# Performance work log

Measured on AMD Instinct MI355X. Metric: run time of the kernel, lower is better.

## Reference

```python
import jax, jax.numpy as jnp
import numpy as np
import math

N_NODES = 100000
N_EDGES = 1600000
IN_DIM = 32
OUT_DIM = 32

def setup_inputs() -> dict:
    key = jax.random.key(0)
    k1, k2, k3, k4 = jax.random.split(key, 4)
    X = jax.random.normal(k1, (N_NODES, IN_DIM), dtype=jnp.float32)
    src_idx = jax.random.randint(k2, (N_EDGES,), 0, N_NODES, dtype=jnp.int64)
    dst_idx = jax.random.randint(k3, (N_EDGES,), 0, N_NODES, dtype=jnp.int64)
    # weights init: uniform(-stdv, stdv), stdv = 1/sqrt(output_dim)
    stdv = 1.0 / math.sqrt(OUT_DIM)
    W = jax.random.uniform(k4, (IN_DIM, OUT_DIM), dtype=jnp.float32,
                           minval=-stdv, maxval=stdv)
    return {"X": X, "W": W, "src_idx": src_idx, "dst_idx": dst_idx}

def reference(X, W, src_idx, dst_idx):
    # GIN sum-aggregation SpMM: agg[i] = sum_{j in N(i)} X[j]
    agg = jax.ops.segment_sum(X[src_idx], dst_idx, num_segments=N_NODES)
    # dense GEMM: X_prime = agg @ W
    return agg @ W
```

## Files before the change

kernel.cpp:

```cpp
#include <hip/hip_runtime.h>

#define N_DIM 32
#define NPB 64
#define NB_FINE_MAX 2048
#define CAPFINE 1280
#define CAPB 48
#define CEPB 16384
#define NSEG_MAX 128
#define FT 512
#define GROWS 512

__device__ __forceinline__ unsigned f2bf_rne(float f) {
    unsigned u = __float_as_uint(f);
    return (u + 0x7FFFu + ((u >> 16) & 1u)) >> 16;
}
__device__ __forceinline__ float bf2f(unsigned h) {
    return __uint_as_float(h << 16);
}

__global__ __launch_bounds__(FT) void k_fused(const float* __restrict__ X,
                                              const float* __restrict__ W,
                                              unsigned* __restrict__ Y,
                                              const int* __restrict__ src,
                                              const int* __restrict__ dst,
                                              int* __restrict__ cnt2,
                                              int* __restrict__ pairs2,
                                              int n_nodes, int n_edges,
                                              int nbins, int nblk_g) {
    __shared__ float Wlds[N_DIM * N_DIM];
    __shared__ int h[NB_FINE_MAX];
    const int t = threadIdx.x;

    if (blockIdx.x < nblk_g) {
        for (int i = t; i < N_DIM * N_DIM; i += FT) Wlds[i] = W[i];
        __syncthreads();
        const int r = blockIdx.x * GROWS + t;
        if (r >= n_nodes) return;

        float x[N_DIM];
        const float4* xr = (const float4*)(X + (size_t)r * N_DIM);
#pragma unroll
        for (int i = 0; i < N_DIM / 4; ++i) {
            float4 v = xr[i];
            x[4 * i + 0] = v.x; x[4 * i + 1] = v.y;
            x[4 * i + 2] = v.z; x[4 * i + 3] = v.w;
        }
        float acc[N_DIM];
#pragma unroll
        for (int c = 0; c < N_DIM; ++c) acc[c] = 0.0f;
#pragma unroll
        for (int k = 0; k < N_DIM; ++k) {
            const float xk = x[k];
#pragma unroll
            for (int c = 0; c < N_DIM; ++c)
                acc[c] = fmaf(xk, Wlds[k * N_DIM + c], acc[c]);
        }
        unsigned yp[16];
#pragma unroll
        for (int q = 0; q < 16; ++q)
            yp[q] = f2bf_rne(acc[2 * q]) | (f2bf_rne(acc[2 * q + 1]) << 16);
        uint4* yr = (uint4*)(Y + (size_t)r * 16);
#pragma unroll
        for (int i = 0; i < 4; ++i)
            yr[i] = make_uint4(yp[4 * i], yp[4 * i + 1],
                               yp[4 * i + 2], yp[4 * i + 3]);
    } else {
        for (int i = t; i < NB_FINE_MAX; i += FT) h[i] = 0;
        __syncthreads();
        const int seg = blockIdx.x - nblk_g;
        const int start = seg * CEPB;
        int* __restrict__ myseg = pairs2 + (size_t)seg * nbins * CAPB;

        for (int kb = 0; kb < CEPB / FT / 8; ++kb) {
            int vw[8], cw[8], rw[8];
#pragma unroll
            for (int k = 0; k < 8; ++k) {
                int e = start + t + (kb * 8 + k) * FT;
                if (e < n_edges) {
                    int d = dst[e];
                    cw[k] = d >> 6;
                    vw[k] = src[e] | ((d & 63) << 17);
                    rw[k] = atomicAdd(&h[cw[k]], 1);
                } else {
                    cw[k] = -1;
                }
            }
#pragma unroll
            for (int k = 0; k < 8; ++k)
                if (cw[k] >= 0 && rw[k] < CAPB)
                    myseg[cw[k] * CAPB + rw[k]] = vw[k];
        }
        __syncthreads();
        for (int i = t; i < nbins; i += FT)
            cnt2[(size_t)seg * nbins + i] = min(h[i], CAPB);
    }
}

__device__ __forceinline__ void addv(float* acc, uint4 v) {
    acc[0] += bf2f(v.x & 0xFFFFu); acc[1] += bf2f(v.x >> 16);
    acc[2] += bf2f(v.y & 0xFFFFu); acc[3] += bf2f(v.y >> 16);
    acc[4] += bf2f(v.z & 0xFFFFu); acc[5] += bf2f(v.z >> 16);
    acc[6] += bf2f(v.w & 0xFFFFu); acc[7] += bf2f(v.w >> 16);
}

__global__ __launch_bounds__(256) void k_agg(const uint4* __restrict__ Y4,
                                             const int* __restrict__ cnt2,
                                             const int* __restrict__ pairs2,
                                             float* __restrict__ out,
                                             int n_nodes, int nbins, int nseg) {
    __shared__ int qbuf[CAPFINE];
    __shared__ int sbin[CAPFINE];
    __shared__ int scnt[NSEG_MAX];
    __shared__ int soff[NSEG_MAX];
    __shared__ int slen;
    __shared__ int cnt[NPB];
    __shared__ int cst[NPB];
    __shared__ int excl[NPB];

    const int t = threadIdx.x;
    const int b = blockIdx.x;

    for (int i = t; i < NSEG_MAX; i += 256)
        scnt[i] = (i < nseg) ? cnt2[(size_t)i * nbins + b] : 0;
    __syncthreads();

    if (t < 64) {
        int a = scnt[t];
        int x = a;
#pragma unroll
        for (int o = 1; o < 64; o <<= 1) {
            int u = __shfl_up(x, o, 64);
            if (t >= o) x += u;
        }
        int b2 = scnt[64 + t];
        int y = b2;
#pragma unroll
        for (int o = 1; o < 64; o <<= 1) {
            int u = __shfl_up(y, o, 64);
            if (t >= o) y += u;
        }
        int tot1 = __shfl(x, 63, 64);
        int tot2 = __shfl(y, 63, 64);
        soff[t] = x - a;
        soff[64 + t] = tot1 + y - b2;
        if (t == 0) slen = tot1 + tot2;
    }
    __syncthreads();
    const int len = min(slen, CAPFINE);

    {
        const int w = t >> 6;
        const int lane = t & 63;
        for (int s = w; s < nseg; s += 4) {
            int c = scnt[s];
            if (lane < c) {
                int p = pairs2[((size_t)s * nbins + b) * CAPB + lane];
                int idx = soff[s] + lane;
                if (idx < CAPFINE) qbuf[idx] = p;
            }
        }
    }
    if (t < NPB) cnt[t] = 0;
    __syncthreads();

    int pv[CAPFINE / 256], rv[CAPFINE / 256];
#pragma unroll
    for (int k = 0; k < CAPFINE / 256; ++k) {
        int i = t + k * 256;
        if (i < len) {
            int p = qbuf[i];
            pv[k] = p;
            rv[k] = atomicAdd(&cnt[(p >> 17) & 63], 1);
        } else {
            pv[k] = -1;
        }
    }
    __syncthreads();
    if (t < 64) {
        int c0 = cnt[t];
        int c = c0;
#pragma unroll
        for (int off = 1; off < 64; off <<= 1) {
            int u = __shfl_up(c, off, 64);
            if (t >= off) c += u;
        }
        cst[t] = c;
        excl[t] = c - c0;
    }
    __syncthreads();
#pragma unroll
    for (int k = 0; k < CAPFINE / 256; ++k) {
        if (pv[k] >= 0) {
            int p = pv[k];
            sbin[excl[(p >> 17) & 63] + rv[k]] = p & 0x1FFFF;
        }
    }
    __syncthreads();

    const int g = t >> 2;
    const int l = t & 3;
    float acc[8];
#pragma unroll
    for (int i = 0; i < 8; ++i) acc[i] = 0.0f;

    const int s1 = cst[g];
    const int s0 = s1 - cnt[g];
    for (int e = s0; e < s1; e += 4) {
        const int m = s1 - e;
        int i0 = sbin[e];
        int i1 = sbin[e + ((m > 1) ? 1 : 0)];
        int i2 = sbin[e + ((m > 2) ? 2 : 0)];
        int i3 = sbin[e + ((m > 3) ? 3 : 0)];
        uint4 v0 = Y4[(size_t)i0 * 4 + l];
        uint4 v1 = Y4[(size_t)i1 * 4 + l];
        uint4 v2 = Y4[(size_t)i2 * 4 + l];
        uint4 v3 = Y4[(size_t)i3 * 4 + l];
        addv(acc, v0);
        if (m > 1) addv(acc, v1);
        if (m > 2) addv(acc, v2);
        if (m > 3) addv(acc, v3);
    }

    const int node = b * NPB + g;
    if (node < n_nodes) {
        ((float4*)out)[(size_t)node * 8 + 2 * l] =
            make_float4(acc[0], acc[1], acc[2], acc[3]);
        ((float4*)out)[(size_t)node * 8 + 2 * l + 1] =
            make_float4(acc[4], acc[5], acc[6], acc[7]);
    }
}

extern "C" void kernel_launch(void* const* d_in, const int* in_sizes, int n_in,
                              void* d_out, int out_size, void* d_ws, size_t ws_size,
                              hipStream_t stream) {
    const float* X   = (const float*)d_in[0];
    const float* W   = (const float*)d_in[1];
    const int*   src = (const int*)d_in[2];
    const int*   dst = (const int*)d_in[3];
    float* out = (float*)d_out;

    const int n_nodes = in_sizes[0] / N_DIM;
    const int n_edges = in_sizes[2];
    const int nbins = (n_nodes + NPB - 1) / NPB;
    const int nseg  = (n_edges + CEPB - 1) / CEPB;

    unsigned* Y  = (unsigned*)d_ws;
    int* cnt2    = (int*)(Y + (size_t)n_nodes * 16);
    int* pairs2  = cnt2 + (size_t)nseg * nbins;

    const int nblk_g = (n_nodes + GROWS - 1) / GROWS;

    k_fused<<<nblk_g + nseg, FT, 0, stream>>>(X, W, Y, src, dst, cnt2, pairs2,
                                              n_nodes, n_edges, nbins, nblk_g);
    k_agg<<<nbins, 256, 0, stream>>>((const uint4*)Y, cnt2, pairs2, out,
                                     n_nodes, nbins, nseg);
}
```

Baseline: 132.6 us.

## Shrink edge segments to raise binning parallelism and gather cells per thread

Edge segments shrink from 16384 to 4096 edges, with per-cell capacity cut from 48 to 16. The binning phase then launches four times as many blocks and each thread handles a single batch of 8 edges. The aggregation kernel now scans up to 512 segment counts in chunks and gathers each segment cell with one thread instead of one wave. This aims to spread the binning pass over more CUs, at the cost of more segment-count reads per bin in the aggregation kernel, serial per-thread gather loops, and a higher chance of cell overflow with capacity 16.

New measurement: 130.9 us. About the same (-1.3%).

```diff
diff --git a/kernel.cpp b/kernel.cpp
--- a/kernel.cpp
+++ b/kernel.cpp
@@ -4,9 +4,9 @@
 #define NPB 64
 #define NB_FINE_MAX 2048
 #define CAPFINE 1280
-#define CAPB 48
-#define CEPB 16384
-#define NSEG_MAX 128
+#define CAPB 16
+#define CEPB 4096
+#define NSEG_PAD 512
 #define FT 512
 #define GROWS 512
 
@@ -65,31 +65,29 @@
             yr[i] = make_uint4(yp[4 * i], yp[4 * i + 1],
                                yp[4 * i + 2], yp[4 * i + 3]);
     } else {
-        for (int i = t; i < NB_FINE_MAX; i += FT) h[i] = 0;
+        for (int i = t; i < nbins; i += FT) h[i] = 0;
         __syncthreads();
         const int seg = blockIdx.x - nblk_g;
         const int start = seg * CEPB;
         int* __restrict__ myseg = pairs2 + (size_t)seg * nbins * CAPB;
 
-        for (int kb = 0; kb < CEPB / FT / 8; ++kb) {
-            int vw[8], cw[8], rw[8];
-#pragma unroll
-            for (int k = 0; k < 8; ++k) {
-                int e = start + t + (kb * 8 + k) * FT;
-                if (e < n_edges) {
-                    int d = dst[e];
-                    cw[k] = d >> 6;
-                    vw[k] = src[e] | ((d & 63) << 17);
-                    rw[k] = atomicAdd(&h[cw[k]], 1);
-                } else {
-                    cw[k] = -1;
-                }
+        int vw[CEPB / FT], cw[CEPB / FT], rw[CEPB / FT];
+#pragma unroll
+        for (int k = 0; k < CEPB / FT; ++k) {
+            int e = start + t + k * FT;
+            if (e < n_edges) {
+                int d = dst[e];
+                cw[k] = d >> 6;
+                vw[k] = src[e] | ((d & 63) << 17);
+                rw[k] = atomicAdd(&h[cw[k]], 1);
+            } else {
+                cw[k] = -1;
             }
-#pragma unroll
-            for (int k = 0; k < 8; ++k)
-                if (cw[k] >= 0 && rw[k] < CAPB)
-                    myseg[cw[k] * CAPB + rw[k]] = vw[k];
-        }
+        }
+#pragma unroll
+        for (int k = 0; k < CEPB / FT; ++k)
+            if (cw[k] >= 0 && rw[k] < CAPB)
+                myseg[(size_t)cw[k] * CAPB + rw[k]] = vw[k];
         __syncthreads();
         for (int i = t; i < nbins; i += FT)
             cnt2[(size_t)seg * nbins + i] = min(h[i], CAPB);
@@ -110,8 +108,8 @@
                                              int n_nodes, int nbins, int nseg) {
     __shared__ int qbuf[CAPFINE];
     __shared__ int sbin[CAPFINE];
-    __shared__ int scnt[NSEG_MAX];
-    __shared__ int soff[NSEG_MAX];
+    __shared__ int scnt[NSEG_PAD];
+    __shared__ int soff[NSEG_PAD];
     __shared__ int slen;
     __shared__ int cnt[NPB];
     __shared__ int cst[NPB];
@@ -120,47 +118,39 @@
     const int t = threadIdx.x;
     const int b = blockIdx.x;
 
-    for (int i = t; i < NSEG_MAX; i += 256)
+    for (int i = t; i < NSEG_PAD; i += 256)
         scnt[i] = (i < nseg) ? cnt2[(size_t)i * nbins + b] : 0;
     __syncthreads();
 
     if (t < 64) {
-        int a = scnt[t];
-        int x = a;
-#pragma unroll
-        for (int o = 1; o < 64; o <<= 1) {
-            int u = __shfl_up(x, o, 64);
-            if (t >= o) x += u;
-        }
-        int b2 = scnt[64 + t];
-        int y = b2;
-#pragma unroll
-        for (int o = 1; o < 64; o <<= 1) {
-            int u = __shfl_up(y, o, 64);
-            if (t >= o) y += u;
-        }
-        int tot1 = __shfl(x, 63, 64);
-        int tot2 = __shfl(y, 63, 64);
-        soff[t] = x - a;
-        soff[64 + t] = tot1 + y - b2;
-        if (t == 0) slen = tot1 + tot2;
-    }
+        int run = 0;
+#pragma unroll
+        for (int ch = 0; ch < NSEG_PAD / 64; ++ch) {
+            int a = scnt[ch * 64 + t];
+            int x = a;
+#pragma unroll
+            for (int o = 1; o < 64; o <<= 1) {
+                int u = __shfl_up(x, o, 64);
+                if (t >= o) x += u;
+            }
+            soff[ch * 64 + t] = run + x - a;
+            run += __shfl(x, 63, 64);
+        }
+        if (t == 0) slen = run;
+    }
+    if (t < NPB) cnt[t] = 0;
     __syncthreads();
     const int len = min(slen, CAPFINE);
 
-    {
-        const int w = t >> 6;
-        const int lane = t & 63;
-        for (int s = w; s < nseg; s += 4) {
-            int c = scnt[s];
-            if (lane < c) {
-                int p = pairs2[((size_t)s * nbins + b) * CAPB + lane];
-                int idx = soff[s] + lane;
-                if (idx < CAPFINE) qbuf[idx] = p;
-            }
-        }
-    }
-    if (t < NPB) cnt[t] = 0;
+    for (int s = t; s < nseg; s += 256) {
+        int c = scnt[s];
+        int o = soff[s];
+        const int* cell = pairs2 + ((size_t)s * nbins + b) * CAPB;
+        for (int j = 0; j < c; ++j) {
+            int idx = o + j;
+            if (idx < CAPFINE) qbuf[idx] = cell[j];
+        }
+    }
     __syncthreads();
 
     int pv[CAPFINE / 256], rv[CAPFINE / 256];
```
